# Kernel optimization log

Hardware: AMD Instinct MI355X
Metric: run time of the kernel (lower is better)

## Reference

```python
import jax, jax.numpy as jnp
import numpy as np

COMMITMENT_COST = 0.25


def setup_inputs() -> dict:
    key = jax.random.key(0)
    k1, k2 = jax.random.split(key)
    inputs = jax.random.normal(k1, (32, 64, 32, 32), dtype=jnp.float32)  # (B, C, H, W)
    embed = jax.random.normal(k2, (64, 1024), dtype=jnp.float32)          # (embedding_dim, num_embeddings)
    return {"inputs": inputs, "embed": embed}


def reference(inputs, embed):
    # Eval-mode forward (EMA buffer updates are training-only side effects).
    B, C, H, W = inputs.shape
    K = embed.shape[1]
    flat = inputs.transpose(0, 2, 3, 1).reshape(-1, C)  # (N, C)
    N = flat.shape[0]

    distances = (jnp.sum(flat * flat, axis=1, keepdims=True)
                 + jnp.sum(embed * embed, axis=0)
                 - 2.0 * flat @ embed)
    encoding_indices = jnp.argmin(distances, axis=1)  # (N,)

    # Gather instead of one-hot @ embed.T (same math, no N x K one-hot)
    quantized = embed.T[encoding_indices]  # (N, C)

    e_latent_loss = jnp.mean((jax.lax.stop_gradient(quantized) - flat) ** 2)
    loss = COMMITMENT_COST * e_latent_loss

    # straight-through estimator
    quantized_st = flat + jax.lax.stop_gradient(quantized - flat)
    quantized_out = quantized_st.reshape(B, H, W, C).transpose(0, 3, 1, 2)

    # avg_probs via scatter-add counts (== mean of one-hot encodings)
    counts = jnp.zeros((K,), dtype=flat.dtype).at[encoding_indices].add(1.0)
    avg_probs = counts / N
    perplexity = jnp.exp(-jnp.sum(avg_probs * jnp.log(avg_probs + 1e-10)))

    return quantized_out, loss, encoding_indices, perplexity
```

## Files before the change

kernel.cpp:

```cpp
#include <hip/hip_runtime.h>

#define N_PIX  32768
#define C_DIM  64
#define K_EMB  1024
#define HW     1024
#define P_TILE 8

#define OUT_Q_OFF    0
#define OUT_LOSS_OFF 2097152
#define OUT_IDX_OFF  2097153
#define OUT_PERP_OFF 2129921


__device__ __forceinline__ unsigned long long pack_score(float d, int k) {
    unsigned int u = __float_as_uint(d);
    u = (u & 0x80000000u) ? ~u : (u | 0x80000000u);
    return ((unsigned long long)u << 32) | (unsigned int)k;
}

__global__ __launch_bounds__(256, 4) void k_main(
    const float* __restrict__ inp, const float* __restrict__ embed,
    unsigned int* __restrict__ counts, float* __restrict__ lossAcc,
    float* __restrict__ out_q, float* __restrict__ out_idx) {
    __shared__ float x_lds[C_DIM * P_TILE];
    __shared__ unsigned long long red[4][P_TILE];
    __shared__ int ksel[P_TILE];
    __shared__ float lred[2];

    const int tid = threadIdx.x;
    const int n0  = blockIdx.x * P_TILE;
    const int b   = n0 >> 10;
    const int hw0 = n0 & 1023;
    const float* __restrict__ xu = inp + b * (C_DIM * HW) + hw0;

    if (tid < 128) {
        const int c  = tid >> 1;
        const int p4 = (tid & 1) * 4;
        *reinterpret_cast<float4*>(&x_lds[c * P_TILE + p4]) =
            *reinterpret_cast<const float4*>(xu + c * HW + p4);
    }
    __syncthreads();

    const int k0 = tid * 4;
    const float4* __restrict__ eb =
        reinterpret_cast<const float4*>(embed) + (k0 >> 2);

    float4 a0 = {0,0,0,0}, a1 = {0,0,0,0}, a2 = {0,0,0,0}, a3 = {0,0,0,0};
    float4 a4 = {0,0,0,0}, a5 = {0,0,0,0}, a6 = {0,0,0,0}, a7 = {0,0,0,0};
    float4 ee = {0,0,0,0};

#define FMA_P(i, xv, E) \
    a##i.x = fmaf((xv), E.x, a##i.x); \
    a##i.y = fmaf((xv), E.y, a##i.y); \
    a##i.z = fmaf((xv), E.z, a##i.z); \
    a##i.w = fmaf((xv), E.w, a##i.w);

#define BODY(E, c) { \
    const float4 xq0 = *reinterpret_cast<const float4*>(&x_lds[(c) * P_TILE + 0]); \
    const float4 xq1 = *reinterpret_cast<const float4*>(&x_lds[(c) * P_TILE + 4]); \
    ee.x = fmaf(E.x, E.x, ee.x); ee.y = fmaf(E.y, E.y, ee.y); \
    ee.z = fmaf(E.z, E.z, ee.z); ee.w = fmaf(E.w, E.w, ee.w); \
    FMA_P(0, xq0.x, E) FMA_P(1, xq0.y, E) FMA_P(2, xq0.z, E) FMA_P(3, xq0.w, E) \
    FMA_P(4, xq1.x, E) FMA_P(5, xq1.y, E) FMA_P(6, xq1.z, E) FMA_P(7, xq1.w, E) }

    float4 E0 = eb[0 * 256], E1 = eb[1 * 256], E2 = eb[2 * 256], E3 = eb[3 * 256];
#pragma unroll 1
    for (int c = 0; c < C_DIM; c += 4) {
        const int cn = (c + 4 < C_DIM) ? (c + 4) : c;
        float4 N0 = eb[(cn + 0) * 256];
        float4 N1 = eb[(cn + 1) * 256];
        float4 N2 = eb[(cn + 2) * 256];
        float4 N3 = eb[(cn + 3) * 256];
        BODY(E0, c + 0)
        BODY(E1, c + 1)
        BODY(E2, c + 2)
        BODY(E3, c + 3)
        E0 = N0; E1 = N1; E2 = N2; E3 = N3;
    }
#undef BODY
#undef FMA_P

    const int wv = tid >> 6, ln = tid & 63;
#define RED_P(i) { \
        const float s0 = fmaf(-2.f, a##i.x, ee.x); \
        const float s1 = fmaf(-2.f, a##i.y, ee.y); \
        const float s2 = fmaf(-2.f, a##i.z, ee.z); \
        const float s3 = fmaf(-2.f, a##i.w, ee.w); \
        unsigned long long m = pack_score(s0, k0), t; \
        t = pack_score(s1, k0 + 1); if (t < m) m = t; \
        t = pack_score(s2, k0 + 2); if (t < m) m = t; \
        t = pack_score(s3, k0 + 3); if (t < m) m = t; \
        for (int off = 32; off > 0; off >>= 1) { \
            unsigned long long o = __shfl_down(m, off, 64); \
            if (o < m) m = o; \
        } \
        if (ln == 0) red[wv][i] = m; }
    RED_P(0) RED_P(1) RED_P(2) RED_P(3)
    RED_P(4) RED_P(5) RED_P(6) RED_P(7)
#undef RED_P

    __syncthreads();
    if (tid < P_TILE) {
        unsigned long long m = red[0][tid];
        if (red[1][tid] < m) m = red[1][tid];
        if (red[2][tid] < m) m = red[2][tid];
        if (red[3][tid] < m) m = red[3][tid];
        const int k = (int)(unsigned int)(m & 0xFFFFFFFFull);
        ksel[tid] = k;
        out_idx[n0 + tid] = (float)k;
        atomicAdd(counts + k, 1u);
    }
    __syncthreads();

    if (tid < 128) {
        const int c  = tid >> 1;
        const int pb = (tid & 1) * 4;
        float ls = 0.f;
        float4 qv;
        float* qvp = &qv.x;
#pragma unroll
        for (int j = 0; j < 4; ++j) {
            const int k = ksel[pb + j];
            const float q  = embed[c * K_EMB + k];
            const float xv = x_lds[c * P_TILE + pb + j];
            const float d  = q - xv;
            ls = fmaf(d, d, ls);
            qvp[j] = q;
        }
        *reinterpret_cast<float4*>(out_q + b * (C_DIM * HW) + c * HW + hw0 + pb) = qv;
        for (int off = 32; off > 0; off >>= 1) ls += __shfl_down(ls, off, 64);
        if (ln == 0) lred[wv] = ls;
    }
    __syncthreads();
    if (tid == 0) atomicAdd(lossAcc, lred[0] + lred[1]);
}

__global__ __launch_bounds__(1024) void k_scalar(
    const unsigned int* __restrict__ counts, const float* __restrict__ lossAcc,
    float* __restrict__ out_loss, float* __restrict__ out_perp) {
    __shared__ float red[16];
    const int tid = threadIdx.x;
    float p = (float)counts[tid] * (1.0f / (float)N_PIX);
    float t = p * logf(p + 1e-10f);
    for (int off = 32; off > 0; off >>= 1) t += __shfl_down(t, off, 64);
    if ((tid & 63) == 0) red[tid >> 6] = t;
    __syncthreads();
    if (tid == 0) {
        float s = 0.f;
#pragma unroll
        for (int i = 0; i < 16; ++i) s += red[i];
        *out_perp = expf(-s);
        *out_loss = 0.25f * (*lossAcc) * (1.0f / (float)(N_PIX * C_DIM));
    }
}

extern "C" void kernel_launch(void* const* d_in, const int* in_sizes, int n_in,
                              void* d_out, int out_size, void* d_ws, size_t ws_size,
                              hipStream_t stream) {
    const float* inp   = (const float*)d_in[0];
    const float* embed = (const float*)d_in[1];
    float* out = (float*)d_out;

    char* ws = (char*)d_ws;
    unsigned int* counts  = (unsigned int*)(ws + 0);
    float*        lossAcc = (float*)(ws + 4096);

    hipMemsetAsync(ws, 0, 4096 + 16, stream);

    k_main<<<dim3(N_PIX / P_TILE), dim3(256), 0, stream>>>(
        inp, embed, counts, lossAcc, out + OUT_Q_OFF, out + OUT_IDX_OFF);
    k_scalar<<<dim3(1), dim3(1024), 0, stream>>>(counts, lossAcc,
        out + OUT_LOSS_OFF, out + OUT_PERP_OFF);
}
```

Measured before the change: 143.6 us.

## Halve block size, double codes per thread, replace global atomics with finalize histogram

k_main now runs 128 threads per block, and each thread scores 8 codes (a low half and a high half of the codebook) for 8 pixels. Each LDS x load is reused across twice as many FMAs, and the x loads are software-pipelined. Global atomics for counts and loss are removed: each block writes a partial loss, and the finalize kernel builds the code histogram in LDS from the written indices. This also drops the memset launch. In exchange there is higher register pressure, with 64 accumulators per thread, and the single-block finalize now reads 32K indices serially.

```diff
diff --git a/kernel.cpp b/kernel.cpp
--- a/kernel.cpp
+++ b/kernel.cpp
@@ -18,12 +18,12 @@
     return ((unsigned long long)u << 32) | (unsigned int)k;
 }
 
-__global__ __launch_bounds__(256, 4) void k_main(
+__global__ __launch_bounds__(128, 4) void k_main(
     const float* __restrict__ inp, const float* __restrict__ embed,
-    unsigned int* __restrict__ counts, float* __restrict__ lossAcc,
-    float* __restrict__ out_q, float* __restrict__ out_idx) {
+    float* __restrict__ lossPart, float* __restrict__ out_q,
+    float* __restrict__ out_idx) {
     __shared__ float x_lds[C_DIM * P_TILE];
-    __shared__ unsigned long long red[4][P_TILE];
+    __shared__ unsigned long long red[2][P_TILE];
     __shared__ int ksel[P_TILE];
     __shared__ float lred[2];
 
@@ -33,7 +33,7 @@
     const int hw0 = n0 & 1023;
     const float* __restrict__ xu = inp + b * (C_DIM * HW) + hw0;
 
-    if (tid < 128) {
+    {
         const int c  = tid >> 1;
         const int p4 = (tid & 1) * 4;
         *reinterpret_cast<float4*>(&x_lds[c * P_TILE + p4]) =
@@ -41,55 +41,72 @@
     }
     __syncthreads();
 
-    const int k0 = tid * 4;
-    const float4* __restrict__ eb =
-        reinterpret_cast<const float4*>(embed) + (k0 >> 2);
+    const int kL = tid * 4;
+    const int kH = 512 + tid * 4;
+    const float4* __restrict__ ebL = reinterpret_cast<const float4*>(embed) + tid;
+    const float4* __restrict__ ebH = ebL + 128;
 
-    float4 a0 = {0,0,0,0}, a1 = {0,0,0,0}, a2 = {0,0,0,0}, a3 = {0,0,0,0};
-    float4 a4 = {0,0,0,0}, a5 = {0,0,0,0}, a6 = {0,0,0,0}, a7 = {0,0,0,0};
-    float4 ee = {0,0,0,0};
+    float4 aL0={0,0,0,0},aL1={0,0,0,0},aL2={0,0,0,0},aL3={0,0,0,0};
+    float4 aL4={0,0,0,0},aL5={0,0,0,0},aL6={0,0,0,0},aL7={0,0,0,0};
+    float4 aH0={0,0,0,0},aH1={0,0,0,0},aH2={0,0,0,0},aH3={0,0,0,0};
+    float4 aH4={0,0,0,0},aH5={0,0,0,0},aH6={0,0,0,0},aH7={0,0,0,0};
+    float4 eeL={0,0,0,0}, eeH={0,0,0,0};
 
-#define FMA_P(i, xv, E) \
-    a##i.x = fmaf((xv), E.x, a##i.x); \
-    a##i.y = fmaf((xv), E.y, a##i.y); \
-    a##i.z = fmaf((xv), E.z, a##i.z); \
-    a##i.w = fmaf((xv), E.w, a##i.w);
+#define FMA8(i, xv, EL, EH) \
+    aL##i.x = fmaf((xv), EL.x, aL##i.x); aL##i.y = fmaf((xv), EL.y, aL##i.y); \
+    aL##i.z = fmaf((xv), EL.z, aL##i.z); aL##i.w = fmaf((xv), EL.w, aL##i.w); \
+    aH##i.x = fmaf((xv), EH.x, aH##i.x); aH##i.y = fmaf((xv), EH.y, aH##i.y); \
+    aH##i.z = fmaf((xv), EH.z, aH##i.z); aH##i.w = fmaf((xv), EH.w, aH##i.w);
 
-#define BODY(E, c) { \
-    const float4 xq0 = *reinterpret_cast<const float4*>(&x_lds[(c) * P_TILE + 0]); \
-    const float4 xq1 = *reinterpret_cast<const float4*>(&x_lds[(c) * P_TILE + 4]); \
-    ee.x = fmaf(E.x, E.x, ee.x); ee.y = fmaf(E.y, E.y, ee.y); \
-    ee.z = fmaf(E.z, E.z, ee.z); ee.w = fmaf(E.w, E.w, ee.w); \
-    FMA_P(0, xq0.x, E) FMA_P(1, xq0.y, E) FMA_P(2, xq0.z, E) FMA_P(3, xq0.w, E) \
-    FMA_P(4, xq1.x, E) FMA_P(5, xq1.y, E) FMA_P(6, xq1.z, E) FMA_P(7, xq1.w, E) }
+#define BODY(EL, EH, A, B) { \
+    eeL.x = fmaf(EL.x, EL.x, eeL.x); eeL.y = fmaf(EL.y, EL.y, eeL.y); \
+    eeL.z = fmaf(EL.z, EL.z, eeL.z); eeL.w = fmaf(EL.w, EL.w, eeL.w); \
+    eeH.x = fmaf(EH.x, EH.x, eeH.x); eeH.y = fmaf(EH.y, EH.y, eeH.y); \
+    eeH.z = fmaf(EH.z, EH.z, eeH.z); eeH.w = fmaf(EH.w, EH.w, eeH.w); \
+    FMA8(0, A.x, EL, EH) FMA8(1, A.y, EL, EH) \
+    FMA8(2, A.z, EL, EH) FMA8(3, A.w, EL, EH) \
+    FMA8(4, B.x, EL, EH) FMA8(5, B.y, EL, EH) \
+    FMA8(6, B.z, EL, EH) FMA8(7, B.w, EL, EH) }
 
-    float4 E0 = eb[0 * 256], E1 = eb[1 * 256], E2 = eb[2 * 256], E3 = eb[3 * 256];
+    float4 EL0 = ebL[0],   EH0 = ebH[0];
+    float4 EL1 = ebL[256], EH1 = ebH[256];
+    float4 XA = *reinterpret_cast<const float4*>(&x_lds[0]);
+    float4 XB = *reinterpret_cast<const float4*>(&x_lds[4]);
+
 #pragma unroll 1
-    for (int c = 0; c < C_DIM; c += 4) {
-        const int cn = (c + 4 < C_DIM) ? (c + 4) : c;
-        float4 N0 = eb[(cn + 0) * 256];
-        float4 N1 = eb[(cn + 1) * 256];
-        float4 N2 = eb[(cn + 2) * 256];
-        float4 N3 = eb[(cn + 3) * 256];
-        BODY(E0, c + 0)
-        BODY(E1, c + 1)
-        BODY(E2, c + 2)
-        BODY(E3, c + 3)
-        E0 = N0; E1 = N1; E2 = N2; E3 = N3;
+    for (int c = 0; c < C_DIM; c += 2) {
+        const int c2 = (c + 2) & 63, c3 = (c + 3) & 63;
+        float4 NL0 = ebL[c2 * 256], NH0 = ebH[c2 * 256];
+        float4 NL1 = ebL[c3 * 256], NH1 = ebH[c3 * 256];
+        const float4 YA = *reinterpret_cast<const float4*>(&x_lds[(c + 1) * P_TILE + 0]);
+        const float4 YB = *reinterpret_cast<const float4*>(&x_lds[(c + 1) * P_TILE + 4]);
+        BODY(EL0, EH0, XA, XB)
+        XA = *reinterpret_cast<const float4*>(&x_lds[c2 * P_TILE + 0]);
+        XB = *reinterpret_cast<const float4*>(&x_lds[c2 * P_TILE + 4]);
+        BODY(EL1, EH1, YA, YB)
+        EL0 = NL0; EH0 = NH0; EL1 = NL1; EH1 = NH1;
     }
 #undef BODY
-#undef FMA_P
+#undef FMA8
 
     const int wv = tid >> 6, ln = tid & 63;
 #define RED_P(i) { \
-        const float s0 = fmaf(-2.f, a##i.x, ee.x); \
-        const float s1 = fmaf(-2.f, a##i.y, ee.y); \
-        const float s2 = fmaf(-2.f, a##i.z, ee.z); \
-        const float s3 = fmaf(-2.f, a##i.w, ee.w); \
-        unsigned long long m = pack_score(s0, k0), t; \
-        t = pack_score(s1, k0 + 1); if (t < m) m = t; \
-        t = pack_score(s2, k0 + 2); if (t < m) m = t; \
-        t = pack_score(s3, k0 + 3); if (t < m) m = t; \
+        const float s0 = fmaf(-2.f, aL##i.x, eeL.x); \
+        const float s1 = fmaf(-2.f, aL##i.y, eeL.y); \
+        const float s2 = fmaf(-2.f, aL##i.z, eeL.z); \
+        const float s3 = fmaf(-2.f, aL##i.w, eeL.w); \
+        const float s4 = fmaf(-2.f, aH##i.x, eeH.x); \
+        const float s5 = fmaf(-2.f, aH##i.y, eeH.y); \
+        const float s6 = fmaf(-2.f, aH##i.z, eeH.z); \
+        const float s7 = fmaf(-2.f, aH##i.w, eeH.w); \
+        unsigned long long m = pack_score(s0, kL), t; \
+        t = pack_score(s1, kL + 1); if (t < m) m = t; \
+        t = pack_score(s2, kL + 2); if (t < m) m = t; \
+        t = pack_score(s3, kL + 3); if (t < m) m = t; \
+        t = pack_score(s4, kH);     if (t < m) m = t; \
+        t = pack_score(s5, kH + 1); if (t < m) m = t; \
+        t = pack_score(s6, kH + 2); if (t < m) m = t; \
+        t = pack_score(s7, kH + 3); if (t < m) m = t; \
         for (int off = 32; off > 0; off >>= 1) { \
             unsigned long long o = __shfl_down(m, off, 64); \
             if (o < m) m = o; \
@@ -103,16 +120,13 @@
     if (tid < P_TILE) {
         unsigned long long m = red[0][tid];
         if (red[1][tid] < m) m = red[1][tid];
-        if (red[2][tid] < m) m = red[2][tid];
-        if (red[3][tid] < m) m = red[3][tid];
         const int k = (int)(unsigned int)(m & 0xFFFFFFFFull);
         ksel[tid] = k;
         out_idx[n0 + tid] = (float)k;
-        atomicAdd(counts + k, 1u);
     }
     __syncthreads();
 
-    if (tid < 128) {
+    {
         const int c  = tid >> 1;
         const int pb = (tid & 1) * 4;
         float ls = 0.f;
@@ -132,25 +146,39 @@
         if (ln == 0) lred[wv] = ls;
     }
     __syncthreads();
-    if (tid == 0) atomicAdd(lossAcc, lred[0] + lred[1]);
+    if (tid == 0) lossPart[blockIdx.x] = lred[0] + lred[1];
 }
 
-__global__ __launch_bounds__(1024) void k_scalar(
-    const unsigned int* __restrict__ counts, const float* __restrict__ lossAcc,
+__global__ __launch_bounds__(1024) void k_fin(
+    const float* __restrict__ out_idx_f, const float* __restrict__ lossPart,
     float* __restrict__ out_loss, float* __restrict__ out_perp) {
-    __shared__ float red[16];
+    __shared__ unsigned int hcnt[K_EMB];
+    __shared__ float redP[16], redL[16];
     const int tid = threadIdx.x;
-    float p = (float)counts[tid] * (1.0f / (float)N_PIX);
+    hcnt[tid] = 0;
+    __syncthreads();
+#pragma unroll
+    for (int i = 0; i < 32; ++i) {
+        const int k = (int)out_idx_f[tid + i * 1024];
+        atomicAdd(&hcnt[k], 1u);
+    }
+    float ls = lossPart[tid] + lossPart[tid + 1024]
+             + lossPart[tid + 2048] + lossPart[tid + 3072];
+    __syncthreads();
+    const float p = (float)hcnt[tid] * (1.0f / (float)N_PIX);
     float t = p * logf(p + 1e-10f);
-    for (int off = 32; off > 0; off >>= 1) t += __shfl_down(t, off, 64);
-    if ((tid & 63) == 0) red[tid >> 6] = t;
+    for (int off = 32; off > 0; off >>= 1) {
+        t  += __shfl_down(t,  off, 64);
+        ls += __shfl_down(ls, off, 64);
+    }
+    if ((tid & 63) == 0) { redP[tid >> 6] = t; redL[tid >> 6] = ls; }
     __syncthreads();
     if (tid == 0) {
-        float s = 0.f;
+        float s = 0.f, L = 0.f;
 #pragma unroll
-        for (int i = 0; i < 16; ++i) s += red[i];
+        for (int i = 0; i < 16; ++i) { s += redP[i]; L += redL[i]; }
         *out_perp = expf(-s);
-        *out_loss = 0.25f * (*lossAcc) * (1.0f / (float)(N_PIX * C_DIM));
+        *out_loss = 0.25f * L * (1.0f / (float)(N_PIX * C_DIM));
     }
 }
 
@@ -160,15 +188,10 @@
     const float* inp   = (const float*)d_in[0];
     const float* embed = (const float*)d_in[1];
     float* out = (float*)d_out;
+    float* lossPart = (float*)d_ws;
 
-    char* ws = (char*)d_ws;
-    unsigned int* counts  = (unsigned int*)(ws + 0);
-    float*        lossAcc = (float*)(ws + 4096);
-
-    hipMemsetAsync(ws, 0, 4096 + 16, stream);
-
-    k_main<<<dim3(N_PIX / P_TILE), dim3(256), 0, stream>>>(
-        inp, embed, counts, lossAcc, out + OUT_Q_OFF, out + OUT_IDX_OFF);
-    k_scalar<<<dim3(1), dim3(1024), 0, stream>>>(counts, lossAcc,
-        out + OUT_LOSS_OFF, out + OUT_PERP_OFF);
+    k_main<<<dim3(N_PIX / P_TILE), dim3(128), 0, stream>>>(
+        inp, embed, lossPart, out + OUT_Q_OFF, out + OUT_IDX_OFF);
+    k_fin<<<dim3(1), dim3(1024), 0, stream>>>(
+        out + OUT_IDX_OFF, lossPart, out + OUT_LOSS_OFF, out + OUT_PERP_OFF);
 }
```

After: 147.0 us. 2.4% more time.
